# Optimization experiments

Hardware: AMD Instinct MI355X
Metric: run time of the kernel (lower is better)

## Reference

```python
import jax, jax.numpy as jnp
import numpy as np
from jax import lax

VOCAB = 32000
EMBED = 1024
HIDDEN = 1024
ML = 64          # config.MAX_LENGTH
L = 50           # input sentence length
HH = HIDDEN // 2 # per-direction encoder hidden


def _lstm_cell(x, h, c, Wih, Whh, bih, bhh):
    # torch LSTM gate order: i, f, g, o
    g = x @ Wih.T + h @ Whh.T + bih + bhh
    i, f, gg, o = jnp.split(g, 4)
    i = jax.nn.sigmoid(i)
    f = jax.nn.sigmoid(f)
    gg = jnp.tanh(gg)
    o = jax.nn.sigmoid(o)
    c = f * c + i * gg
    return o * jnp.tanh(c), c


def setup_inputs() -> dict:
    key = jax.random.key(0)
    ks = jax.random.split(key, 24)
    def n(k, shape, s=0.05):
        return jax.random.normal(k, shape, jnp.float32) * s
    return {
        "x_tokens": jax.random.randint(ks[0], (L,), 0, VOCAB, jnp.int32),
        "allowed_mask": jnp.ones((VOCAB + ML,), jnp.float32),
        "embedding": n(ks[1], (VOCAB, EMBED)),
        # encoder bi-LSTM (two cells, each hidden//2)
        "Wih_f": n(ks[2], (4 * HH, EMBED)), "Whh_f": n(ks[3], (4 * HH, HH)),
        "bih_f": n(ks[4], (4 * HH,)), "bhh_f": n(ks[5], (4 * HH,)),
        "Wih_b": n(ks[6], (4 * HH, EMBED)), "Whh_b": n(ks[7], (4 * HH, HH)),
        "bih_b": n(ks[8], (4 * HH,)), "bhh_b": n(ks[9], (4 * HH,)),
        # decoder LSTM: input = embed + 2*hidden
        "Wih_d": n(ks[10], (4 * HIDDEN, EMBED + 2 * HIDDEN)),
        "Whh_d": n(ks[11], (4 * HIDDEN, HIDDEN)),
        "bih_d": n(ks[12], (4 * HIDDEN,)), "bhh_d": n(ks[13], (4 * HIDDEN,)),
        # attention: Linear(2*hidden -> MAX_LENGTH)
        "attn_W": n(ks[14], (ML, 2 * HIDDEN)), "attn_b": n(ks[15], (ML,)),
        # generate layer: Linear(hidden -> vocab)
        "gen_W": n(ks[16], (VOCAB, HIDDEN)), "gen_b": n(ks[17], (VOCAB,)),
        # copy layer: Linear(hidden -> hidden)
        "copy_W": n(ks[18], (HIDDEN, HIDDEN)), "copy_b": n(ks[19], (HIDDEN,)),
    }


def _forward(allowed_mask, embedding, Wih_f, Whh_f, bih_f, bhh_f,
             Wih_b, Whh_b, bih_b, bhh_b, Wih_d, Whh_d, bih_d, bhh_d,
             attn_W, attn_b, gen_W, gen_b, copy_W, copy_b, x_tokens):
    xemb = embedding[x_tokens]  # (L, EMBED)

    # --- encoder: two LSTM cells both stepped forward-in-time (as in the
    # original, where the bidirectional LSTM is called one token at a time) ---
    def enc_step(carry, xe):
        hf, cf, hb, cb = carry
        hf, cf = _lstm_cell(xe, hf, cf, Wih_f, Whh_f, bih_f, bhh_f)
        hb, cb = _lstm_cell(xe, hb, cb, Wih_b, Whh_b, bih_b, bhh_b)
        return (hf, cf, hb, cb), jnp.concatenate([hf, hb])

    z = jnp.zeros((HH,), xemb.dtype)
    (hf, cf, hb, cb), enc = lax.scan(enc_step, (z, z, z, z), xemb)
    enc_outs = jnp.zeros((ML, HIDDEN), xemb.dtype).at[:L].set(enc)  # padded buffer
    h0 = jnp.concatenate([hf, hb])  # (HIDDEN,) decoder init
    c0 = jnp.concatenate([cf, cb])

    copy_enc = jnp.tanh(enc_outs @ copy_W.T + copy_b)  # (ML, HIDDEN), loop-invariant
    pos = jnp.arange(ML)
    sent_pad = jnp.full((ML,), -1, jnp.int32).at[:L].set(x_tokens)
    sos_emb = embedding[0]

    def dec_step(carry, t):
        h, c, prev_probs, prev_word, dec_in = carry
        first = t == 0
        # attentive read
        a = jnp.concatenate([dec_in, h])  # (2*HIDDEN,)
        attw = jax.nn.softmax(a @ attn_W.T + attn_b)
        attentive = attw @ enc_outs  # (HIDDEN,)
        # selective (copy) read from previous step's copy probs
        pc = prev_probs[VOCAB:]
        m = ((pos >= 1) & (pos < L - 1) & (sent_pad != prev_word)).astype(pc.dtype)
        pc = pc * m
        s = pc.sum()
        pc = jnp.where(s > 0, pc / jnp.where(s > 0, s, 1.0), pc)
        selective = pc @ enc_outs
        zero = jnp.zeros_like(attentive)
        attentive = jnp.where(first, zero, attentive)
        selective = jnp.where(first, zero, selective)
        # decoder LSTM step
        h, c = _lstm_cell(jnp.concatenate([dec_in, selective, attentive]),
                          h, c, Wih_d, Whh_d, bih_d, bhh_d)
        gen = h @ gen_W.T + gen_b        # (VOCAB,)
        copy = copy_enc @ h              # (ML,)
        probs = jax.nn.softmax(jnp.concatenate([gen, copy]))
        dist = probs * allowed_mask
        # deterministic action (argmax in place of Categorical.sample)
        aidx = jnp.argmax(dist)
        is_voc = aidx < VOCAB
        src = sent_pad[jnp.clip(aidx - VOCAB, 0, L - 1)]
        action = jnp.where(is_voc, aidx, src).astype(jnp.int32)
        prob = dist[aidx] + jnp.where(
            is_voc, jnp.zeros((), dist.dtype), dist[jnp.clip(action, 0, VOCAB - 1)])
        new = (h, c, lax.stop_gradient(probs), action, embedding[action])
        return new, (h, prob, action)

    carry0 = (h0, c0, jnp.zeros((VOCAB + ML,), h0.dtype),
              jnp.array(-1, jnp.int32), sos_emb)
    _, (hs, probs, actions) = lax.scan(dec_step, carry0, jnp.arange(ML))
    states = jnp.concatenate([h0[None], hs])  # (ML+1, HIDDEN)
    return states, probs, actions


def reference(x_tokens, allowed_mask, embedding, Wih_f, Whh_f, bih_f, bhh_f,
              Wih_b, Whh_b, bih_b, bhh_b, Wih_d, Whh_d, bih_d, bhh_d,
              attn_W, attn_b, gen_W, gen_b, copy_W, copy_b):
    return _forward(allowed_mask, embedding, Wih_f, Whh_f, bih_f, bhh_f,
                    Wih_b, Whh_b, bih_b, bhh_b, Wih_d, Whh_d, bih_d, bhh_d,
                    attn_W, attn_b, gen_W, gen_b, copy_W, copy_b, x_tokens)
```

## Files before the change

kernel.cpp:

```cpp
#include <hip/hip_runtime.h>
#include <math.h>

#define L 50
#define ML 64
#define VOCAB 32000
#define EMBED 1024
#define HID 1024
#define HH 512
#define TOT (VOCAB+ML)
#define NPART 501

#define WS_ENC_GATES 0
#define WS_C_ENC     8192
#define WS_ENC_OUTS  10240
#define WS_COPY_ENC  75776
#define WS_H_DEC     141312
#define WS_C_DEC     143360
#define WS_X_DEC     145408
#define WS_DGATES    148480
#define WS_LOGITS    152576
#define WS_PARTS     184640
#define WS_ATTW      186688
#define WS_PC        186752
#define WS_G         186816
#define WS_G_END     (186816+8192*64)

__device__ __forceinline__ float wred_sum(float v){
  #pragma unroll
  for(int o=32;o;o>>=1) v += __shfl_xor(v,o,64);
  return v;
}
__device__ __forceinline__ float wred_max(float v){
  #pragma unroll
  for(int o=32;o;o>>=1) v = fmaxf(v,__shfl_xor(v,o,64));
  return v;
}
__device__ __forceinline__ float sigm(float x){ return 1.0f/(1.0f+__expf(-x)); }
__device__ __forceinline__ float d4(float4 a, float4 b){ return a.x*b.x + a.y*b.y + a.z*b.z + a.w*b.w; }

__global__ __launch_bounds__(256) void k_enc_step(
  const int* __restrict__ xt, const float* __restrict__ emb,
  const float* __restrict__ Wih_f, const float* __restrict__ Whh_f,
  const float* __restrict__ bih_f, const float* __restrict__ bhh_f,
  const float* __restrict__ Wih_b, const float* __restrict__ Whh_b,
  const float* __restrict__ bih_b, const float* __restrict__ bhh_b,
  float* __restrict__ ws, int t)
{
  __shared__ __align__(16) float h_lds[1024];
  __shared__ __align__(16) float xe[1024];
  const int tid = threadIdx.x;
  float* gates   = ws + WS_ENC_GATES;
  float* c_enc   = ws + WS_C_ENC;
  float* enc_outs= ws + WS_ENC_OUTS;
  {
    const int tok = xt[t];
    const float* er = emb + (size_t)tok*EMBED;
    for(int j=tid;j<1024;j+=256) xe[j]=er[j];
  }
  if(t>0){
    const float* gp = gates + ((t-1)&1)*4096;
    const float* cp = c_enc + (t&1)*1024;
    float* cw = c_enc + ((t-1)&1)*1024;
    for(int u=tid;u<1024;u+=256){
      int base=(u<512)?0:2048, uu=(u<512)?u:(u-512);
      float ig=gp[base+uu], fg=gp[base+512+uu], gg=gp[base+1024+uu], og=gp[base+1536+uu];
      float cprev=(t==1)?0.0f:cp[u];
      float c=sigm(fg)*cprev+sigm(ig)*tanhf(gg);
      float h=sigm(og)*tanhf(c);
      h_lds[u]=h;
      if(blockIdx.x==0){ cw[u]=c; enc_outs[(size_t)(t-1)*1024+u]=h; }
    }
  }
  __syncthreads();
  float* gw = gates + (t&1)*4096;
  const int wave=tid>>6, lane=tid&63;
  for(int rr=0;rr<2;rr++){
    int r=blockIdx.x*8+wave*2+rr;
    bool isF=(r<2048); int rl=isF?r:(r-2048);
    const float* Wih=isF?Wih_f:Wih_b;
    const float* Whh=isF?Whh_f:Whh_b;
    float bias=isF?(bih_f[rl]+bhh_f[rl]):(bih_b[rl]+bhh_b[rl]);
    const float* wr=Wih+(size_t)rl*EMBED;
    float acc=0.0f;
    #pragma unroll
    for(int c4=0;c4<4;c4++){
      int m=c4*256+lane*4;
      acc += d4(*(const float4*)(wr+m), *(const float4*)(&xe[m]));
    }
    if(t>0){
      const float* hr=Whh+(size_t)rl*HH;
      const float* hs=&h_lds[isF?0:512];
      #pragma unroll
      for(int c2=0;c2<2;c2++){
        int m=c2*256+lane*4;
        acc += d4(*(const float4*)(hr+m), *(const float4*)(&hs[m]));
      }
    }
    acc=wred_sum(acc);
    if(lane==0) gw[r]=acc+bias;
  }
}

__global__ __launch_bounds__(256) void k_copy_final(
  const float* __restrict__ emb,
  const float* __restrict__ copy_W, const float* __restrict__ copy_b,
  float* __restrict__ ws, float* __restrict__ out)
{
  __shared__ __align__(16) float hf[1024];
  const int tid=threadIdx.x, b=blockIdx.x, wave=tid>>6, lane=tid&63;
  float* gates = ws + WS_ENC_GATES;
  float* c_enc = ws + WS_C_ENC;
  float* enc_outs = ws + WS_ENC_OUTS;
  float* cenc = ws + WS_COPY_ENC;
  float* h_dec = ws + WS_H_DEC;
  float* c_dec = ws + WS_C_DEC;
  float* x_dec = ws + WS_X_DEC;
  {
    const float* gp = gates + ((L-1)&1)*4096;
    const float* cp = c_enc + ((L-2)&1)*1024;
    for(int u=tid;u<1024;u+=256){
      int base=(u<512)?0:2048, uu=(u<512)?u:(u-512);
      float ig=gp[base+uu], fg=gp[base+512+uu], gg=gp[base+1024+uu], og=gp[base+1536+uu];
      float c=sigm(fg)*cp[u]+sigm(ig)*tanhf(gg);
      float h=sigm(og)*tanhf(c);
      hf[u]=h;
      if(b==0){
        enc_outs[(size_t)(L-1)*1024+u]=h;
        h_dec[1024+u]=h;
        c_dec[1024+u]=c;
        out[u]=h;
      }
    }
    if(b==1) for(int j=tid;j<(ML-L)*1024;j+=256) enc_outs[(size_t)L*1024+j]=0.0f;
    if(b==2) for(int j=tid;j<1024;j+=256){
      x_dec[j]=emb[j];
      x_dec[1024+j]=0.0f;
      x_dec[2048+j]=0.0f;
    }
  }
  __syncthreads();
  int j = b*4 + wave;
  const float* wr = copy_W + (size_t)j*1024;
  float4 w0=*(const float4*)(wr+0*256+lane*4);
  float4 w1=*(const float4*)(wr+1*256+lane*4);
  float4 w2=*(const float4*)(wr+2*256+lane*4);
  float4 w3=*(const float4*)(wr+3*256+lane*4);
  float bj = copy_b[j];
  for(int k=0;k<L-1;k++){
    const float* er = enc_outs + (size_t)k*1024;
    float acc = d4(w0,*(const float4*)(er+0*256+lane*4))
              + d4(w1,*(const float4*)(er+1*256+lane*4))
              + d4(w2,*(const float4*)(er+2*256+lane*4))
              + d4(w3,*(const float4*)(er+3*256+lane*4));
    acc = wred_sum(acc);
    if(lane==0) cenc[(size_t)k*1024+j]=tanhf(acc+bj);
  }
  {
    float acc = d4(w0,*(const float4*)(&hf[0*256+lane*4]))
              + d4(w1,*(const float4*)(&hf[1*256+lane*4]))
              + d4(w2,*(const float4*)(&hf[2*256+lane*4]))
              + d4(w3,*(const float4*)(&hf[3*256+lane*4]));
    acc = wred_sum(acc);
    if(lane==0) cenc[(size_t)(L-1)*1024+j]=tanhf(acc+bj);
  }
  if(lane==0){
    float z=tanhf(0.0f+bj);
    for(int k=L;k<ML;k++) cenc[(size_t)k*1024+j]=z;
  }
}

__global__ __launch_bounds__(256) void k_gmat(const float* __restrict__ Wih_d, float* __restrict__ ws)
{
  __shared__ __align__(16) float elds[16*1024];
  const int tid=threadIdx.x, wave=tid>>6, lane=tid&63;
  const float* enc = ws + WS_ENC_OUTS;
  float* G = ws + WS_G;
  float4 w[4][4];
  int rg[4];
  #pragma unroll
  for(int q=0;q<4;q++){
    int r = blockIdx.x*16 + wave*4 + q;
    rg[q]=r;
    const float* W = (r<4096) ? (Wih_d + (size_t)r*3072 + 1024)
                              : (Wih_d + (size_t)(r-4096)*3072 + 2048);
    #pragma unroll
    for(int c4=0;c4<4;c4++) w[q][c4]=*(const float4*)(W + c4*256 + lane*4);
  }
  for(int chunk=0;chunk<4;chunk++){
    __syncthreads();
    for(int idx=tid; idx<16*1024; idx+=256) elds[idx]=enc[(size_t)chunk*16*1024+idx];
    __syncthreads();
    for(int k=0;k<16;k++){
      #pragma unroll
      for(int q=0;q<4;q++){
        float acc=0.0f;
        #pragma unroll
        for(int c4=0;c4<4;c4++)
          acc += d4(w[q][c4], *(const float4*)(&elds[k*1024 + c4*256 + lane*4]));
        acc=wred_sum(acc);
        if(lane==0) G[(size_t)rg[q]*64 + chunk*16 + k]=acc;
      }
    }
  }
}

__global__ __launch_bounds__(1024) void k_fin(
  const int* __restrict__ xt, const float* __restrict__ amask,
  const float* __restrict__ emb,
  const float* __restrict__ attn_W, const float* __restrict__ attn_b,
  float* __restrict__ ws, float* __restrict__ out, int t, int fin_only)
{
  __shared__ __align__(16) float dec_in[1024];
  __shared__ __align__(16) float hprev[1024];
  __shared__ float r_lm[1024], r_sm[1024], r_ky[1024];
  __shared__ int r_ix[1024];
  __shared__ float attw_raw[64];
  __shared__ float s_lmax, s_Z;
  __shared__ int s_act;
  const int tid=threadIdx.x, wave=tid>>6, lane=tid&63;
  float* h_dec=ws+WS_H_DEC; float* x_dec=ws+WS_X_DEC;
  float* logits=ws+WS_LOGITS; float* parts=ws+WS_PARTS;
  float* aww=ws+WS_ATTW; float* pcw=ws+WS_PC;

  if(t==0){
    for(int j=tid;j<1024;j+=1024) x_dec[j]=emb[j];
    if(tid<64){ aww[tid]=0.0f; pcw[tid]=0.0f; }
    return;
  }
  {
    float lm=-1e30f, sm=0.0f, ky=-1e30f; int ix=0x7fffffff;
    if(tid<NPART){
      const float4 p = *(const float4*)(parts+(size_t)tid*4);
      lm=p.x; sm=p.y; ky=p.z; ix=__float_as_int(p.w);
    }
    r_lm[tid]=lm; r_sm[tid]=sm; r_ky[tid]=ky; r_ix[tid]=ix;
    __syncthreads();
    for(int s=512;s;s>>=1){
      if(tid<s){
        float blm=r_lm[tid+s], bsm=r_sm[tid+s];
        float alm=r_lm[tid], a_sm=r_sm[tid];
        if(blm>alm){ r_sm[tid]=a_sm*__expf(alm-blm)+bsm; r_lm[tid]=blm; }
        else r_sm[tid]=a_sm+bsm*__expf(blm-alm);
        float bky=r_ky[tid+s]; int bix=r_ix[tid+s];
        if(bky>r_ky[tid] || (bky==r_ky[tid] && bix<r_ix[tid])){ r_ky[tid]=bky; r_ix[tid]=bix; }
      }
      __syncthreads();
    }
    if(tid==0){
      float lmax=r_lm[0], Z=r_sm[0];
      int aidx=(r_ky[0]<=-1e29f)?0:r_ix[0];
      bool isv=(aidx<VOCAB);
      int kcl=aidx-VOCAB; kcl=kcl<0?0:(kcl>(L-1)?(L-1):kcl);
      int sp=xt[kcl];
      int action=isv?aidx:sp;
      float prob=amask[aidx]*__expf(logits[aidx]-lmax)/Z;
      if(!isv){
        int a2=action<0?0:(action>(VOCAB-1)?(VOCAB-1):action);
        prob += amask[a2]*__expf(logits[a2]-lmax)/Z;
      }
      out[65*1024 + (t-1)] = prob;
      out[65*1024 + 64 + (t-1)] = (float)action;
      s_lmax=lmax; s_Z=Z; s_act=action;
    }
  }
  __syncthreads();
  if(fin_only) return;

  const int action=s_act;
  if(tid<64){
    int k=tid;
    float v=__expf(logits[VOCAB+k]-s_lmax)/s_Z;
    int sp=(k<L)? xt[k] : -1;
    float m=(k>=1 && k<(L-1) && sp!=action)?1.0f:0.0f;
    float pv=v*m;
    float s=wred_sum(pv);
    pcw[k]=(s>0.0f)? pv/s : pv;
  }
  {
    int row = action<0 ? action+VOCAB : action;
    const float* er = emb + (size_t)row*EMBED;
    const float* hp = h_dec + ((t-1)&1)*1024;
    for(int j=tid;j<1024;j+=1024){
      float v=er[j];
      dec_in[j]=v; hprev[j]=hp[j];
      x_dec[j]=v;
    }
  }
  __syncthreads();
  for(int rr=0;rr<4;rr++){
    int r=wave*4+rr;
    const float* wr = attn_W + (size_t)r*2048;
    float acc=0.0f;
    #pragma unroll
    for(int c4=0;c4<4;c4++){
      int m=c4*256+lane*4;
      acc += d4(*(const float4*)(wr+m),      *(const float4*)(&dec_in[m]));
      acc += d4(*(const float4*)(wr+1024+m), *(const float4*)(&hprev[m]));
    }
    acc=wred_sum(acc);
    if(lane==0) attw_raw[r]=acc+attn_b[r];
  }
  __syncthreads();
  if(tid<64){
    float v=attw_raw[tid];
    float mx=wred_max(v);
    float e=__expf(v-mx);
    float s=wred_sum(e);
    aww[tid]=e/s;
  }
}

__global__ __launch_bounds__(256) void k_dec_gates2(
  const float* __restrict__ Wih_d, const float* __restrict__ Whh_d,
  const float* __restrict__ bih_d, const float* __restrict__ bhh_d,
  float* __restrict__ ws, int t)
{
  __shared__ __align__(16) float di[1024];
  __shared__ __align__(16) float hh[1024];
  __shared__ float pcs[64], aws[64];
  const int tid=threadIdx.x;
  float* x_dec=ws+WS_X_DEC; float* h_dec=ws+WS_H_DEC; float* dg=ws+WS_DGATES;
  const float* G=ws+WS_G;
  for(int j=tid;j<1024;j+=256) di[j]=x_dec[j];
  {
    const float* hp=h_dec+((t+1)&1)*1024;
    for(int j=tid;j<1024;j+=256) hh[j]=hp[j];
  }
  if(tid<64){ pcs[tid]=(ws+WS_PC)[tid]; aws[tid]=(ws+WS_ATTW)[tid]; }
  __syncthreads();
  const int wave=tid>>6, lane=tid&63;
  for(int rr=0;rr<2;rr++){
    int r=blockIdx.x*8+wave*2+rr;
    const float* wd=Wih_d+(size_t)r*3072;
    float acc=0.0f;
    #pragma unroll
    for(int c4=0;c4<4;c4++){
      int m=c4*256+lane*4;
      acc += d4(*(const float4*)(wd+m), *(const float4*)(&di[m]));
    }
    const float* hr=Whh_d+(size_t)r*1024;
    #pragma unroll
    for(int c4=0;c4<4;c4++){
      int m=c4*256+lane*4;
      acc += d4(*(const float4*)(hr+m), *(const float4*)(&hh[m]));
    }
    acc += G[(size_t)r*64+lane]*pcs[lane];
    acc += G[(size_t)(4096+r)*64+lane]*aws[lane];
    acc=wred_sum(acc);
    if(lane==0) dg[r]=acc+bih_d[r]+bhh_d[r];
  }
}

__global__ __launch_bounds__(256) void k_dec_init(const float* __restrict__ emb, float* __restrict__ ws)
{
  float* x_dec=ws+WS_X_DEC;
  for(int j=threadIdx.x;j<1024;j+=256){
    x_dec[j]=emb[j];
    x_dec[1024+j]=0.0f;
    x_dec[2048+j]=0.0f;
  }
}

__global__ __launch_bounds__(256) void k_attn(
  const int* __restrict__ xt, const float* __restrict__ amask,
  const float* __restrict__ emb,
  const float* __restrict__ attn_W, const float* __restrict__ attn_b,
  float* __restrict__ ws, float* __restrict__ out, int t, int fin_only)
{
  __shared__ __align__(16) float dec_in[1024];
  __shared__ __align__(16) float hprev[1024];
  __shared__ float r_lm[256], r_sm[256], r_ky[256];
  __shared__ int r_ix[256];
  __shared__ float s_lmax, s_Z;
  __shared__ int s_act;
  const int tid=threadIdx.x;
  float* h_dec=ws+WS_H_DEC; float* x_dec=ws+WS_X_DEC;
  float* logits=ws+WS_LOGITS; float* parts=ws+WS_PARTS;
  float* attw_raw=ws+WS_ATTW; float* pcw=ws+WS_PC;
  {
    float lm=-INFINITY, sm=0.0f, ky=-INFINITY; int ix=0x7fffffff;
    for(int i=tid;i<NPART;i+=256){
      const float4 p = *(const float4*)(parts+(size_t)i*4);
      float plm=p.x, psm=p.y, pky=p.z; int pix=__float_as_int(p.w);
      if(plm>lm){ sm = sm*__expf(lm-plm)+psm; lm=plm; }
      else sm += psm*__expf(plm-lm);
      if(pky>ky || (pky==ky && pix<ix)){ ky=pky; ix=pix; }
    }
    r_lm[tid]=lm; r_sm[tid]=sm; r_ky[tid]=ky; r_ix[tid]=ix;
    __syncthreads();
    for(int s=128;s;s>>=1){
      if(tid<s){
        float blm=r_lm[tid+s], bsm=r_sm[tid+s];
        float alm=r_lm[tid], a_sm=r_sm[tid];
        if(blm>alm){ r_sm[tid]=a_sm*__expf(alm-blm)+bsm; r_lm[tid]=blm; }
        else r_sm[tid]=a_sm+bsm*__expf(blm-alm);
        float bky=r_ky[tid+s]; int bix=r_ix[tid+s];
        if(bky>r_ky[tid] || (bky==r_ky[tid] && bix<r_ix[tid])){ r_ky[tid]=bky; r_ix[tid]=bix; }
      }
      __syncthreads();
    }
    if(tid==0){
      float lmax=r_lm[0]; float Z=r_sm[0];
      float bky=r_ky[0];
      int aidx = (bky==-INFINITY)?0:r_ix[0];
      bool isv = aidx<VOCAB;
      int kcl = aidx-VOCAB; kcl = kcl<0?0:(kcl>(L-1)?(L-1):kcl);
      int sp = xt[kcl];
      int action = isv? aidx : sp;
      if(blockIdx.x==0){
        float prob = amask[aidx]*__expf(logits[aidx]-lmax)/Z;
        if(!isv){
          int a2 = action<0?0:(action>(VOCAB-1)?(VOCAB-1):action);
          prob += amask[a2]*__expf(logits[a2]-lmax)/Z;
        }
        out[65*1024 + (t-1)] = prob;
        out[65*1024 + 64 + (t-1)] = (float)action;
      }
      s_lmax=lmax; s_Z=Z; s_act=action;
    }
  }
  __syncthreads();
  if(fin_only) return;
  const int action = s_act;
  if(blockIdx.x==0 && tid<64){
    int k=tid;
    float v=__expf(logits[VOCAB+k]-s_lmax)/s_Z;
    int sp=(k<L)? xt[k] : -1;
    float m=(k>=1 && k<(L-1) && sp!=action)?1.0f:0.0f;
    float pv=v*m;
    float s=wred_sum(pv);
    pcw[k]=(s>0.0f)? pv/s : pv;
  }
  {
    int row = action<0 ? action+VOCAB : action;
    const float* er = emb + (size_t)row*EMBED;
    const float* hp = h_dec + ((t-1)&1)*1024;
    for(int j=tid;j<1024;j+=256){
      float v=er[j];
      dec_in[j]=v; hprev[j]=hp[j];
      if(blockIdx.x==0) x_dec[j]=v;
    }
  }
  __syncthreads();
  if(tid<64){
    const int lane=tid;
    const float* wr = attn_W + (size_t)blockIdx.x*2048;
    float acc=0.0f;
    #pragma unroll
    for(int c4=0;c4<4;c4++){
      int m=c4*256+lane*4;
      acc += d4(*(const float4*)(wr+m),      *(const float4*)(&dec_in[m]));
      acc += d4(*(const float4*)(wr+1024+m), *(const float4*)(&hprev[m]));
    }
    acc=wred_sum(acc);
    if(lane==0) attw_raw[blockIdx.x]=acc+attn_b[blockIdx.x];
  }
}

__global__ __launch_bounds__(256) void k_prep(float* __restrict__ ws)
{
  __shared__ float attw_s[64], pc_s[64];
  const int tid=threadIdx.x;
  float* enc_outs=ws+WS_ENC_OUTS; float* x_dec=ws+WS_X_DEC;
  float* attw_raw=ws+WS_ATTW; float* pcw=ws+WS_PC;
  if(tid<64){
    float v=attw_raw[tid];
    float mx=wred_max(v);
    float e=__expf(v-mx);
    float s=wred_sum(e);
    attw_s[tid]=e/s;
    pc_s[tid]=pcw[tid];
  }
  __syncthreads();
  int j=blockIdx.x*256+tid;
  float aA=0.0f, aS=0.0f;
  for(int k=0;k<ML;k++){
    float e=enc_outs[(size_t)k*1024+j];
    aA += attw_s[k]*e;
    aS += pc_s[k]*e;
  }
  x_dec[1024+j]=aS;
  x_dec[2048+j]=aA;
}

__global__ __launch_bounds__(256) void k_dec_gates(
  const float* __restrict__ Wih_d, const float* __restrict__ Whh_d,
  const float* __restrict__ bih_d, const float* __restrict__ bhh_d,
  float* __restrict__ ws, int t)
{
  __shared__ __align__(16) float x_lds[4096];
  const int tid=threadIdx.x;
  float* x_dec=ws+WS_X_DEC; float* h_dec=ws+WS_H_DEC; float* dg=ws+WS_DGATES;
  for(int j=tid;j<3072;j+=256) x_lds[j]=x_dec[j];
  {
    const float* hp=h_dec+((t+1)&1)*1024;
    for(int j=tid;j<1024;j+=256) x_lds[3072+j]=hp[j];
  }
  __syncthreads();
  const int wave=tid>>6, lane=tid&63;
  for(int rr=0;rr<2;rr++){
    int r=blockIdx.x*8+wave*2+rr;
    const float* wr=Wih_d+(size_t)r*3072;
    float acc=0.0f;
    #pragma unroll
    for(int c4=0;c4<12;c4++){
      int m=c4*256+lane*4;
      acc += d4(*(const float4*)(wr+m), *(const float4*)(&x_lds[m]));
    }
    const float* hr=Whh_d+(size_t)r*1024;
    #pragma unroll
    for(int c4=0;c4<4;c4++){
      int m=c4*256+lane*4;
      acc += d4(*(const float4*)(hr+m), *(const float4*)(&x_lds[3072+m]));
    }
    acc=wred_sum(acc);
    if(lane==0) dg[r]=acc+bih_d[r]+bhh_d[r];
  }
}

__global__ __launch_bounds__(256) void k_dec_gen(
  const float* __restrict__ gen_W, const float* __restrict__ gen_b,
  const float* __restrict__ amask,
  float* __restrict__ ws, float* __restrict__ out, int t)
{
  __shared__ __align__(16) float h_lds[1024];
  __shared__ float w_lm[4], w_sm[4], w_ky[4];
  __shared__ int w_ix[4];
  const int tid=threadIdx.x;
  float* dg=ws+WS_DGATES;
  float* c_dec=ws+WS_C_DEC; float* h_dec=ws+WS_H_DEC;
  float* logits=ws+WS_LOGITS; float* parts=ws+WS_PARTS;
  float* cenc=ws+WS_COPY_ENC;
  {
    const float* cp=c_dec+((t+1)&1)*1024;
    float* cw=c_dec+(t&1)*1024;
    float* hw=h_dec+(t&1)*1024;
    for(int u=tid;u<1024;u+=256){
      float ig=dg[u], fg=dg[1024+u], gg=dg[2048+u], og=dg[3072+u];
      float c=sigm(fg)*cp[u]+sigm(ig)*tanhf(gg);
      float h=sigm(og)*tanhf(c);
      h_lds[u]=h;
      if(blockIdx.x==0){ cw[u]=c; hw[u]=h; out[(size_t)(t+1)*1024+u]=h; }
    }
  }
  __syncthreads();
  const int wave=tid>>6, lane=tid&63;
  const int b=blockIdx.x;
  const bool isGen=(b<500);
  const int rbase = isGen ? (b*64+wave*16) : (VOCAB+wave*16);
  float lv[16];
  #pragma unroll
  for(int rr=0;rr<16;rr++){
    const float* wr = isGen ? gen_W+(size_t)(rbase+rr)*1024
                            : cenc +(size_t)(rbase-VOCAB+rr)*1024;
    float acc=0.0f;
    #pragma unroll
    for(int c4=0;c4<4;c4++){
      int m=c4*256+lane*4;
      acc += d4(*(const float4*)(wr+m), *(const float4*)(&h_lds[m]));
    }
    acc=wred_sum(acc);
    lv[rr] = isGen ? acc+gen_b[rbase+rr] : acc;
  }
  if(lane==0){
    float lm=-INFINITY, ky=-INFINITY; int ix=0;
    #pragma unroll
    for(int rr=0;rr<16;rr++){
      int gi=rbase+rr;
      logits[gi]=lv[rr];
      lm=fmaxf(lm,lv[rr]);
      float mk=amask[gi];
      float kk = (mk>0.0f)? (lv[rr]+__logf(mk)) : -INFINITY;
      if(kk>ky){ ky=kk; ix=gi; }
    }
    float sm=0.0f;
    #pragma unroll
    for(int rr=0;rr<16;rr++) sm += __expf(lv[rr]-lm);
    w_lm[wave]=lm; w_sm[wave]=sm; w_ky[wave]=ky; w_ix[wave]=ix;
  }
  __syncthreads();
  if(tid==0){
    float lm=w_lm[0], sm=w_sm[0], ky=w_ky[0]; int ix=w_ix[0];
    for(int w=1;w<4;w++){
      float blm=w_lm[w], bsm=w_sm[w];
      if(blm>lm){ sm=sm*__expf(lm-blm)+bsm; lm=blm; }
      else sm += bsm*__expf(blm-lm);
      if(w_ky[w]>ky || (w_ky[w]==ky && w_ix[w]<ix)){ ky=w_ky[w]; ix=w_ix[w]; }
    }
    float4 p; p.x=lm; p.y=sm; p.z=ky; p.w=__int_as_float(ix);
    *(float4*)(parts+(size_t)blockIdx.x*4)=p;
  }
}

extern "C" void kernel_launch(void* const* d_in, const int* in_sizes, int n_in,
                              void* d_out, int out_size, void* d_ws, size_t ws_size,
                              hipStream_t stream)
{
  const int*   xt     = (const int*)d_in[0];
  const float* amask  = (const float*)d_in[1];
  const float* emb    = (const float*)d_in[2];
  const float* Wih_f  = (const float*)d_in[3];
  const float* Whh_f  = (const float*)d_in[4];
  const float* bih_f  = (const float*)d_in[5];
  const float* bhh_f  = (const float*)d_in[6];
  const float* Wih_b  = (const float*)d_in[7];
  const float* Whh_b  = (const float*)d_in[8];
  const float* bih_b  = (const float*)d_in[9];
  const float* bhh_b  = (const float*)d_in[10];
  const float* Wih_d  = (const float*)d_in[11];
  const float* Whh_d  = (const float*)d_in[12];
  const float* bih_d  = (const float*)d_in[13];
  const float* bhh_d  = (const float*)d_in[14];
  const float* attn_W = (const float*)d_in[15];
  const float* attn_b = (const float*)d_in[16];
  const float* gen_W  = (const float*)d_in[17];
  const float* gen_b  = (const float*)d_in[18];
  const float* copy_W = (const float*)d_in[19];
  const float* copy_b = (const float*)d_in[20];
  float* out=(float*)d_out;
  float* ws =(float*)d_ws;

  for(int t=0;t<L;t++)
    k_enc_step<<<512,256,0,stream>>>(xt,emb,Wih_f,Whh_f,bih_f,bhh_f,Wih_b,Whh_b,bih_b,bhh_b,ws,t);
  k_copy_final<<<256,256,0,stream>>>(emb,copy_W,copy_b,ws,out);

  const bool big = ws_size >= (size_t)WS_G_END*sizeof(float);
  if(big){
    k_gmat<<<512,256,0,stream>>>(Wih_d,ws);
    for(int t=0;t<ML;t++){
      k_fin       <<<1,1024,0,stream>>>(xt,amask,emb,attn_W,attn_b,ws,out,t,0);
      k_dec_gates2<<<512,256,0,stream>>>(Wih_d,Whh_d,bih_d,bhh_d,ws,t);
      k_dec_gen   <<<501,256,0,stream>>>(gen_W,gen_b,amask,ws,out,t);
    }
    k_fin<<<1,1024,0,stream>>>(xt,amask,emb,attn_W,attn_b,ws,out,ML,1);
  } else {
    k_dec_init<<<1,256,0,stream>>>(emb,ws);
    k_dec_gates<<<512,256,0,stream>>>(Wih_d,Whh_d,bih_d,bhh_d,ws,0);
    k_dec_gen  <<<501,256,0,stream>>>(gen_W,gen_b,amask,ws,out,0);
    for(int t=1;t<ML;t++){
      k_attn     <<<64,256,0,stream>>>(xt,amask,emb,attn_W,attn_b,ws,out,t,0);
      k_prep     <<<4,256,0,stream>>>(ws);
      k_dec_gates<<<512,256,0,stream>>>(Wih_d,Whh_d,bih_d,bhh_d,ws,t);
      k_dec_gen  <<<501,256,0,stream>>>(gen_W,gen_b,amask,ws,out,t);
    }
    k_attn<<<1,256,0,stream>>>(xt,amask,emb,attn_W,attn_b,ws,out,ML,1);
  }
}
```

Before: 3.540 ms.

## Hoist encoder input projections out of recurrence and split decoder finalize kernel

Precomputes the encoder input-to-gate projections for all 50 tokens in one kernel, so each recurrent step only multiplies the small hidden-to-hidden weights. The decoder finalize kernel is spread over 16 blocks of 256 threads instead of one 1024-thread block, with the attention softmax moved into the gates kernel and the chosen action passed through the workspace. This takes the large input weight reads off the sequential critical path and parallelises the attention matvec, at the cost of more workspace and redundant argmax reduction in every block.

```diff
diff --git a/kernel.cpp b/kernel.cpp
--- a/kernel.cpp
+++ b/kernel.cpp
@@ -22,8 +22,11 @@
 #define WS_PARTS     184640
 #define WS_ATTW      186688
 #define WS_PC        186752
-#define WS_G         186816
-#define WS_G_END     (186816+8192*64)
+#define WS_ACT       186816
+#define WS_G         186880
+#define WS_G_END     (186880+8192*64)
+#define WS_PREG      711168
+#define WS_END       (711168+50*4096)
 
 __device__ __forceinline__ float wred_sum(float v){
   #pragma unroll
@@ -37,6 +40,86 @@
 }
 __device__ __forceinline__ float sigm(float x){ return 1.0f/(1.0f+__expf(-x)); }
 __device__ __forceinline__ float d4(float4 a, float4 b){ return a.x*b.x + a.y*b.y + a.z*b.z + a.w*b.w; }
+
+__global__ __launch_bounds__(256) void k_enc_pre2(
+  const int* __restrict__ xt, const float* __restrict__ emb,
+  const float* __restrict__ Wih_f, const float* __restrict__ bih_f, const float* __restrict__ bhh_f,
+  const float* __restrict__ Wih_b, const float* __restrict__ bih_b, const float* __restrict__ bhh_b,
+  float* __restrict__ ws)
+{
+  __shared__ int toks[L];
+  const int tid=threadIdx.x, b=blockIdx.x, wave=tid>>6, lane=tid&63;
+  float* pg = ws + WS_PREG;
+  if(tid<L) toks[tid]=xt[tid];
+  float4 wih[2][4]; float bias[2];
+  #pragma unroll
+  for(int rr=0;rr<2;rr++){
+    int r=b*8+wave*2+rr; bool isF=(r<2048); int rl=isF?r:(r-2048);
+    const float* wp=(isF?Wih_f:Wih_b)+(size_t)rl*EMBED;
+    #pragma unroll
+    for(int c4=0;c4<4;c4++) wih[rr][c4]=*(const float4*)(wp+c4*256+lane*4);
+    bias[rr]= isF?(bih_f[rl]+bhh_f[rl]):(bih_b[rl]+bhh_b[rl]);
+  }
+  __syncthreads();
+  for(int t=0;t<L;t++){
+    const float* er = emb + (size_t)toks[t]*EMBED;
+    #pragma unroll
+    for(int rr=0;rr<2;rr++){
+      int r=b*8+wave*2+rr;
+      float acc=0.0f;
+      #pragma unroll
+      for(int c4=0;c4<4;c4++) acc += d4(wih[rr][c4], *(const float4*)(er + c4*256 + lane*4));
+      acc=wred_sum(acc);
+      if(lane==0) pg[(size_t)t*4096+r]=acc+bias[rr];
+    }
+  }
+}
+
+__global__ __launch_bounds__(256) void k_enc_rec(
+  const float* __restrict__ Whh_f, const float* __restrict__ Whh_b,
+  float* __restrict__ ws, int t)
+{
+  __shared__ __align__(16) float h_lds[1024];
+  const int tid=threadIdx.x, b=blockIdx.x, wave=tid>>6, lane=tid&63;
+  float* gates   = ws + WS_ENC_GATES;
+  float* c_enc   = ws + WS_C_ENC;
+  float* enc_outs= ws + WS_ENC_OUTS;
+  const float* pg = ws + WS_PREG + (size_t)t*4096;
+  if(t>0){
+    const float* gp = gates + ((t-1)&1)*4096;
+    const float* cp = c_enc + (t&1)*1024;
+    float* cw = c_enc + ((t-1)&1)*1024;
+    for(int u=tid;u<1024;u+=256){
+      int base=(u<512)?0:2048, uu=(u<512)?u:(u-512);
+      float ig=gp[base+uu], fg=gp[base+512+uu], gg=gp[base+1024+uu], og=gp[base+1536+uu];
+      float cprev=(t==1)?0.0f:cp[u];
+      float c=sigm(fg)*cprev+sigm(ig)*tanhf(gg);
+      float h=sigm(og)*tanhf(c);
+      h_lds[u]=h;
+      if(b==0){ cw[u]=c; enc_outs[(size_t)(t-1)*1024+u]=h; }
+    }
+  }
+  __syncthreads();
+  float* gw = gates + (t&1)*4096;
+  #pragma unroll
+  for(int rr=0;rr<2;rr++){
+    int r=b*8+wave*2+rr; bool isF=(r<2048); int rl=isF?r:(r-2048);
+    if(t==0){
+      if(lane==0) gw[r]=pg[r];
+    } else {
+      const float* hr=(isF?Whh_f:Whh_b)+(size_t)rl*HH;
+      const float* hs=&h_lds[isF?0:512];
+      float acc=0.0f;
+      #pragma unroll
+      for(int c2=0;c2<2;c2++){
+        int m=c2*256+lane*4;
+        acc += d4(*(const float4*)(hr+m), *(const float4*)(&hs[m]));
+      }
+      acc=wred_sum(acc);
+      if(lane==0) gw[r]=pg[r]+acc;
+    }
+  }
+}
 
 __global__ __launch_bounds__(256) void k_enc_step(
   const int* __restrict__ xt, const float* __restrict__ emb,
@@ -204,7 +287,7 @@
   }
 }
 
-__global__ __launch_bounds__(1024) void k_fin(
+__global__ __launch_bounds__(256) void k_fin16(
   const int* __restrict__ xt, const float* __restrict__ amask,
   const float* __restrict__ emb,
   const float* __restrict__ attn_W, const float* __restrict__ attn_b,
@@ -212,30 +295,27 @@
 {
   __shared__ __align__(16) float dec_in[1024];
   __shared__ __align__(16) float hprev[1024];
-  __shared__ float r_lm[1024], r_sm[1024], r_ky[1024];
-  __shared__ int r_ix[1024];
-  __shared__ float attw_raw[64];
+  __shared__ float r_lm[256], r_sm[256], r_ky[256];
+  __shared__ int r_ix[256];
   __shared__ float s_lmax, s_Z;
   __shared__ int s_act;
-  const int tid=threadIdx.x, wave=tid>>6, lane=tid&63;
-  float* h_dec=ws+WS_H_DEC; float* x_dec=ws+WS_X_DEC;
+  const int tid=threadIdx.x, b=blockIdx.x, wave=tid>>6, lane=tid&63;
+  float* h_dec=ws+WS_H_DEC;
   float* logits=ws+WS_LOGITS; float* parts=ws+WS_PARTS;
-  float* aww=ws+WS_ATTW; float* pcw=ws+WS_PC;
-
-  if(t==0){
-    for(int j=tid;j<1024;j+=1024) x_dec[j]=emb[j];
-    if(tid<64){ aww[tid]=0.0f; pcw[tid]=0.0f; }
-    return;
-  }
-  {
-    float lm=-1e30f, sm=0.0f, ky=-1e30f; int ix=0x7fffffff;
-    if(tid<NPART){
-      const float4 p = *(const float4*)(parts+(size_t)tid*4);
-      lm=p.x; sm=p.y; ky=p.z; ix=__float_as_int(p.w);
+  float* attw_raw=ws+WS_ATTW; float* pcw=ws+WS_PC;
+
+  {
+    float lm=-INFINITY, sm=0.0f, ky=-INFINITY; int ix=0x7fffffff;
+    for(int i=tid;i<NPART;i+=256){
+      const float4 p = *(const float4*)(parts+(size_t)i*4);
+      float plm=p.x, psm=p.y, pky=p.z; int pix=__float_as_int(p.w);
+      if(plm>lm){ sm = sm*__expf(lm-plm)+psm; lm=plm; }
+      else sm += psm*__expf(plm-lm);
+      if(pky>ky || (pky==ky && pix<ix)){ ky=pky; ix=pix; }
     }
     r_lm[tid]=lm; r_sm[tid]=sm; r_ky[tid]=ky; r_ix[tid]=ix;
     __syncthreads();
-    for(int s=512;s;s>>=1){
+    for(int s=128;s;s>>=1){
       if(tid<s){
         float blm=r_lm[tid+s], bsm=r_sm[tid+s];
         float alm=r_lm[tid], a_sm=r_sm[tid];
@@ -247,27 +327,31 @@
       __syncthreads();
     }
     if(tid==0){
-      float lmax=r_lm[0], Z=r_sm[0];
-      int aidx=(r_ky[0]<=-1e29f)?0:r_ix[0];
-      bool isv=(aidx<VOCAB);
-      int kcl=aidx-VOCAB; kcl=kcl<0?0:(kcl>(L-1)?(L-1):kcl);
-      int sp=xt[kcl];
-      int action=isv?aidx:sp;
-      float prob=amask[aidx]*__expf(logits[aidx]-lmax)/Z;
-      if(!isv){
-        int a2=action<0?0:(action>(VOCAB-1)?(VOCAB-1):action);
-        prob += amask[a2]*__expf(logits[a2]-lmax)/Z;
+      float lmax=r_lm[0]; float Z=r_sm[0];
+      float bky=r_ky[0];
+      int aidx = (bky==-INFINITY)?0:r_ix[0];
+      bool isv = aidx<VOCAB;
+      int kcl = aidx-VOCAB; kcl = kcl<0?0:(kcl>(L-1)?(L-1):kcl);
+      int sp = xt[kcl];
+      int action = isv? aidx : sp;
+      if(b==0){
+        float prob = amask[aidx]*__expf(logits[aidx]-lmax)/Z;
+        if(!isv){
+          int a2 = action<0?0:(action>(VOCAB-1)?(VOCAB-1):action);
+          prob += amask[a2]*__expf(logits[a2]-lmax)/Z;
+        }
+        out[65*1024 + (t-1)] = prob;
+        out[65*1024 + 64 + (t-1)] = (float)action;
+        *(int*)(ws+WS_ACT) = action;
       }
-      out[65*1024 + (t-1)] = prob;
-      out[65*1024 + 64 + (t-1)] = (float)action;
       s_lmax=lmax; s_Z=Z; s_act=action;
     }
   }
   __syncthreads();
   if(fin_only) return;
 
-  const int action=s_act;
-  if(tid<64){
+  const int action = s_act;
+  if(b==0 && tid<64){
     int k=tid;
     float v=__expf(logits[VOCAB+k]-s_lmax)/s_Z;
     int sp=(k<L)? xt[k] : -1;
@@ -280,15 +364,11 @@
     int row = action<0 ? action+VOCAB : action;
     const float* er = emb + (size_t)row*EMBED;
     const float* hp = h_dec + ((t-1)&1)*1024;
-    for(int j=tid;j<1024;j+=1024){
-      float v=er[j];
-      dec_in[j]=v; hprev[j]=hp[j];
-      x_dec[j]=v;
-    }
-  }
-  __syncthreads();
-  for(int rr=0;rr<4;rr++){
-    int r=wave*4+rr;
+    for(int j=tid;j<1024;j+=256){ dec_in[j]=er[j]; hprev[j]=hp[j]; }
+  }
+  __syncthreads();
+  {
+    int r = b*4 + wave;
     const float* wr = attn_W + (size_t)r*2048;
     float acc=0.0f;
     #pragma unroll
@@ -300,17 +380,10 @@
     acc=wred_sum(acc);
     if(lane==0) attw_raw[r]=acc+attn_b[r];
   }
-  __syncthreads();
-  if(tid<64){
-    float v=attw_raw[tid];
-    float mx=wred_max(v);
-    float e=__expf(v-mx);
-    float s=wred_sum(e);
-    aww[tid]=e/s;
-  }
-}
-
-__global__ __launch_bounds__(256) void k_dec_gates2(
+}
+
+__global__ __launch_bounds__(256) void k_dec_gates3(
+  const float* __restrict__ emb,
   const float* __restrict__ Wih_d, const float* __restrict__ Whh_d,
   const float* __restrict__ bih_d, const float* __restrict__ bhh_d,
   float* __restrict__ ws, int t)
@@ -319,14 +392,28 @@
   __shared__ __align__(16) float hh[1024];
   __shared__ float pcs[64], aws[64];
   const int tid=threadIdx.x;
-  float* x_dec=ws+WS_X_DEC; float* h_dec=ws+WS_H_DEC; float* dg=ws+WS_DGATES;
+  float* h_dec=ws+WS_H_DEC; float* dg=ws+WS_DGATES;
   const float* G=ws+WS_G;
-  for(int j=tid;j<1024;j+=256) di[j]=x_dec[j];
+  if(t==0){
+    for(int j=tid;j<1024;j+=256) di[j]=emb[j];
+    if(tid<64){ pcs[tid]=0.0f; aws[tid]=0.0f; }
+  } else {
+    const int action = *(const int*)(ws+WS_ACT);
+    const float* er = emb + (size_t)action*EMBED;
+    for(int j=tid;j<1024;j+=256) di[j]=er[j];
+    if(tid<64){
+      pcs[tid]=(ws+WS_PC)[tid];
+      float v=(ws+WS_ATTW)[tid];
+      float mx=wred_max(v);
+      float e=__expf(v-mx);
+      float s=wred_sum(e);
+      aws[tid]=e/s;
+    }
+  }
   {
     const float* hp=h_dec+((t+1)&1)*1024;
     for(int j=tid;j<1024;j+=256) hh[j]=hp[j];
   }
-  if(tid<64){ pcs[tid]=(ws+WS_PC)[tid]; aws[tid]=(ws+WS_ATTW)[tid]; }
   __syncthreads();
   const int wave=tid>>6, lane=tid&63;
   for(int rr=0;rr<2;rr++){
@@ -620,19 +707,29 @@
   float* out=(float*)d_out;
   float* ws =(float*)d_ws;
 
-  for(int t=0;t<L;t++)
-    k_enc_step<<<512,256,0,stream>>>(xt,emb,Wih_f,Whh_f,bih_f,bhh_f,Wih_b,Whh_b,bih_b,bhh_b,ws,t);
+  const bool hasG    = ws_size >= (size_t)WS_G_END*sizeof(float);
+  const bool hasPreg = ws_size >= (size_t)WS_END*sizeof(float);
+
+  if(hasPreg){
+    k_enc_pre2<<<512,256,0,stream>>>(xt,emb,Wih_f,bih_f,bhh_f,Wih_b,bih_b,bhh_b,ws);
+    for(int t=0;t<L;t++)
+      k_enc_rec<<<512,256,0,stream>>>(Whh_f,Whh_b,ws,t);
+  } else {
+    for(int t=0;t<L;t++)
+      k_enc_step<<<512,256,0,stream>>>(xt,emb,Wih_f,Whh_f,bih_f,bhh_f,Wih_b,Whh_b,bih_b,bhh_b,ws,t);
+  }
   k_copy_final<<<256,256,0,stream>>>(emb,copy_W,copy_b,ws,out);
 
-  const bool big = ws_size >= (size_t)WS_G_END*sizeof(float);
-  if(big){
+  if(hasG){
     k_gmat<<<512,256,0,stream>>>(Wih_d,ws);
-    for(int t=0;t<ML;t++){
-      k_fin       <<<1,1024,0,stream>>>(xt,amask,emb,attn_W,attn_b,ws,out,t,0);
-      k_dec_gates2<<<512,256,0,stream>>>(Wih_d,Whh_d,bih_d,bhh_d,ws,t);
+    k_dec_gates3<<<512,256,0,stream>>>(emb,Wih_d,Whh_d,bih_d,bhh_d,ws,0);
+    k_dec_gen   <<<501,256,0,stream>>>(gen_W,gen_b,amask,ws,out,0);
+    for(int t=1;t<ML;t++){
+      k_fin16     <<<16,256,0,stream>>>(xt,amask,emb,attn_W,attn_b,ws,out,t,0);
+      k_dec_gates3<<<512,256,0,stream>>>(emb,Wih_d,Whh_d,bih_d,bhh_d,ws,t);
       k_dec_gen   <<<501,256,0,stream>>>(gen_W,gen_b,amask,ws,out,t);
     }
-    k_fin<<<1,1024,0,stream>>>(xt,amask,emb,attn_W,attn_b,ws,out,ML,1);
+    k_fin16<<<1,256,0,stream>>>(xt,amask,emb,attn_W,attn_b,ws,out,ML,1);
   } else {
     k_dec_init<<<1,256,0,stream>>>(emb,ws);
     k_dec_gates<<<512,256,0,stream>>>(Wih_d,Whh_d,bih_d,bhh_d,ws,0);
```

Result: faster. 3.099 ms (-12.5%).
